# Optimization experiments

Hardware: AMD Instinct MI355X
Metric: run time of the kernel (lower is better)

The kernel has to match this reference:

```python
import jax, jax.numpy as jnp
import numpy as np

NUM_HEADS = 16
KEY_SIZE = 64
MODEL = NUM_HEADS * KEY_SIZE
B, S = 4, 2048
NEG = jnp.float32(-1e9)


def alibi_bidirectional_bias(num_heads, seq_len):
    # slopes for num_heads//2 heads: 1 / x**(i+1), x = 24**(1/h)
    h = num_heads // 2
    x = 24.0 ** (1.0 / h)
    slopes = (1.0 / x ** jnp.arange(1, h + 1, dtype=jnp.float32))[:, None, None]  # [h,1,1]
    i = jnp.arange(seq_len)
    rel = (i[None, :] - i[:, None]).astype(jnp.float32)  # rel[i,j] = j - i
    # forward (causal): tril(j - i) + (-1e9 strictly above diag)
    fwd = slopes * jnp.tril(rel) + jnp.triu(jnp.full((seq_len, seq_len), NEG), k=1)
    # backward (anti-causal): triu(i - j) + (-1e9 strictly below diag)
    bwd = slopes * jnp.triu(-rel) + jnp.tril(jnp.full((seq_len, seq_len), NEG), k=-1)
    return jnp.concatenate([fwd, bwd], axis=0)  # [num_heads, S, S]


def setup_inputs() -> dict:
    key = jax.random.key(0)
    ks = jax.random.split(key, 11)
    sc = 0.02
    d = {
        "query": jax.random.normal(ks[0], (B, S, MODEL), jnp.float32),
        "key": jax.random.normal(ks[1], (B, S, MODEL), jnp.float32),
        "value": jax.random.normal(ks[2], (B, S, MODEL), jnp.float32),
        "Wq": jax.random.normal(ks[3], (MODEL, MODEL), jnp.float32) * sc,
        "bq": jnp.zeros((MODEL,), jnp.float32),
        "Wk": jax.random.normal(ks[4], (MODEL, MODEL), jnp.float32) * sc,
        "bk": jnp.zeros((MODEL,), jnp.float32),
        "Wv": jax.random.normal(ks[5], (MODEL, MODEL), jnp.float32) * sc,
        "bv": jnp.zeros((MODEL,), jnp.float32),
        "Wo": jax.random.normal(ks[6], (MODEL, MODEL), jnp.float32) * sc,
        "bo": jnp.zeros((MODEL,), jnp.float32),
    }
    return d


def reference(query, key, value, Wq, bq, Wk, bk, Wv, bv, Wo, bo):
    b, s, _ = query.shape
    H, D = NUM_HEADS, KEY_SIZE

    def proj(x, W, bias):
        return (x @ W.T + bias).reshape(b, s, H, D).transpose(0, 2, 1, 3)  # [B,H,S,D]

    q = proj(query, Wq, bq)
    k = proj(key, Wk, bk)
    v = proj(value, Wv, bv)

    bias = alibi_bidirectional_bias(H, s)  # [H,S,S], broadcasts over batch
    scores = jnp.einsum("bhqd,bhkd->bhqk", q, k) / jnp.sqrt(jnp.float32(D)) + bias
    attn = jax.nn.softmax(scores, axis=-1)
    out = jnp.einsum("bhqk,bhkd->bhqd", attn, v)
    out = out.transpose(0, 2, 1, 3).reshape(b, s, H * D)
    return out @ Wo.T + bo
```

## Files before the change

kernel.cpp:

```cpp
#include <hip/hip_runtime.h>
#include <hip/hip_bf16.h>
#include <stdint.h>

typedef unsigned short u16;
typedef __attribute__((ext_vector_type(8))) __bf16 bf16x8;
typedef __attribute__((ext_vector_type(4))) float f32x4;
typedef __attribute__((ext_vector_type(4))) unsigned int u32x4;

#define S_LEN 2048
#define NHEAD 16
#define HDIM 64
#define DMODEL 1024
#define NBATCH 4
#define MTOK (NBATCH * S_LEN)

__device__ __forceinline__ u16 f2bf(float f) {
    uint32_t u = __float_as_uint(f);
    u += 0x7fffu + ((u >> 16) & 1u);
    return (u16)(u >> 16);
}

__device__ __forceinline__ void gld_lds16(const u16* g, u16* l) {
    __builtin_amdgcn_global_load_lds(
        (const __attribute__((address_space(1))) void*)g,
        (__attribute__((address_space(3))) void*)l, 16, 0, 0);
}

__global__ __launch_bounds__(256) void cast_all(
        const float* __restrict__ q, const float* __restrict__ k, const float* __restrict__ v,
        const float* __restrict__ wq, const float* __restrict__ wk,
        const float* __restrict__ wv, const float* __restrict__ wo,
        u16* __restrict__ xq, u16* __restrict__ xk, u16* __restrict__ xv,
        u16* __restrict__ wqb, u16* __restrict__ wkb, u16* __restrict__ wvb,
        u16* __restrict__ wob) {
    size_t idx4 = (size_t)blockIdx.x * 256 + threadIdx.x;
    const float* src;
    u16* dst;
    size_t off;
    if (idx4 < (size_t)3 << 21) {
        int t = (int)(idx4 >> 21);
        off = (idx4 & ((1u << 21) - 1)) * 4;
        src = (t == 0) ? q : (t == 1) ? k : v;
        dst = (t == 0) ? xq : (t == 1) ? xk : xv;
    } else {
        size_t w = idx4 - ((size_t)3 << 21);
        int t = (int)(w >> 18);
        off = (w & ((1u << 18) - 1)) * 4;
        src = (t == 0) ? wq : (t == 1) ? wk : (t == 2) ? wv : wo;
        dst = (t == 0) ? wqb : (t == 1) ? wkb : (t == 2) ? wvb : wob;
    }
    float4 val = *(const float4*)(src + off);
    ushort4 o;
    o.x = f2bf(val.x); o.y = f2bf(val.y); o.z = f2bf(val.z); o.w = f2bf(val.w);
    *(ushort4*)(dst + off) = o;
}

#define TM 128
#define TN 128

__device__ __forceinline__ void gemm_body(const u16* __restrict__ A,
                                          const u16* __restrict__ W,
                                          const float* __restrict__ bias,
                                          void* __restrict__ outp, int mode,
                                          int m0, int n0) {
    __shared__ __align__(16) u16 As[TM * 32];
    __shared__ __align__(16) u16 Bs[TN * 32];
    const int tid  = threadIdx.x;
    const int lane = tid & 63;
    const int wv   = tid >> 6;
    const int l16  = lane & 15;
    const int quad = lane >> 4;
    const int wm   = (wv >> 1) * 64;
    const int wn   = (wv & 1) * 64;

    f32x4 acc[4][4];
#pragma unroll
    for (int i = 0; i < 4; i++)
#pragma unroll
        for (int j = 0; j < 4; j++) acc[i][j] = {};

    const int arow = wv * 16 + (lane >> 2);
    const int acol = (lane & 3) * 8;
    const u16* gA = A + (size_t)(m0 + arow) * DMODEL + acol;
    const u16* gB = W + (size_t)(n0 + arow) * DMODEL + acol;
    u16* lA = As + wv * 16 * 32;
    u16* lB = Bs + wv * 16 * 32;

    for (int kb = 0; kb < DMODEL; kb += 32) {
        gld_lds16(gA + kb, lA);
        gld_lds16(gA + kb + (size_t)64 * DMODEL, lA + 64 * 32);
        gld_lds16(gB + kb, lB);
        gld_lds16(gB + kb + (size_t)64 * DMODEL, lB + 64 * 32);
        __builtin_amdgcn_s_waitcnt(0x0F70);
        __syncthreads();

        bf16x8 af[4], bfv[4];
#pragma unroll
        for (int i = 0; i < 4; i++)
            af[i] = *(const bf16x8*)(&As[(wm + i * 16 + l16) * 32 + quad * 8]);
#pragma unroll
        for (int j = 0; j < 4; j++)
            bfv[j] = *(const bf16x8*)(&Bs[(wn + j * 16 + l16) * 32 + quad * 8]);
#pragma unroll
        for (int i = 0; i < 4; i++)
#pragma unroll
            for (int j = 0; j < 4; j++)
                acc[i][j] = __builtin_amdgcn_mfma_f32_16x16x32_bf16(af[i], bfv[j], acc[i][j], 0, 0, 0);
        __syncthreads();
    }

#pragma unroll
    for (int j = 0; j < 4; j++) {
        int n = n0 + wn + j * 16 + l16;
        float bv = bias[n];
#pragma unroll
        for (int i = 0; i < 4; i++) {
            int mbase = m0 + wm + i * 16 + quad * 4;
#pragma unroll
            for (int r = 0; r < 4; r++) {
                int m = mbase + r;
                float v = acc[i][j][r] + bv;
                if (mode == 2) {
                    ((float*)outp)[(size_t)m * DMODEL + n] = v;
                } else {
                    int b = m >> 11, s = m & (S_LEN - 1);
                    int h = n >> 6, d = n & 63;
                    u16* o = (u16*)outp;
                    size_t idx = (mode == 0)
                        ? ((((size_t)(b * NHEAD + h)) * S_LEN + s) * HDIM + d)
                        : ((((size_t)(b * NHEAD + h)) * HDIM + d) * S_LEN + s);
                    o[idx] = f2bf(v);
                }
            }
        }
    }
}

__device__ __forceinline__ void gemm_coords(int& m0, int& n0) {
    const int lid = blockIdx.x + 8 * blockIdx.y;
    const int xcd = lid & 7;
    const int s   = lid >> 3;
    n0 = (s & 7) * TN;
    m0 = ((s >> 3) + 8 * xcd) * TM;
}

__global__ __launch_bounds__(256) void gemm_qkv(
        const u16* __restrict__ xq, const u16* __restrict__ xk, const u16* __restrict__ xv,
        const u16* __restrict__ wq, const u16* __restrict__ wk, const u16* __restrict__ wv,
        const float* __restrict__ bq, const float* __restrict__ bk, const float* __restrict__ bv,
        u16* __restrict__ Qb, u16* __restrict__ Kb, u16* __restrict__ Vb) {
    int z = blockIdx.z;
    const u16* A   = (z == 0) ? xq : (z == 1) ? xk : xv;
    const u16* W   = (z == 0) ? wq : (z == 1) ? wk : wv;
    const float* b = (z == 0) ? bq : (z == 1) ? bk : bv;
    u16* out       = (z == 0) ? Qb : (z == 1) ? Kb : Vb;
    int m0, n0;
    gemm_coords(m0, n0);
    gemm_body(A, W, b, out, (z == 2) ? 1 : 0, m0, n0);
}

__global__ __launch_bounds__(256) void gemm_one(
        const u16* __restrict__ A, const u16* __restrict__ W,
        const float* __restrict__ bias, void* __restrict__ out, int mode) {
    int m0, n0;
    gemm_coords(m0, n0);
    gemm_body(A, W, bias, out, mode, m0, n0);
}

__global__ __launch_bounds__(256, 4) void flash_kernel(
        const u16* __restrict__ Q, const u16* __restrict__ K,
        const u16* __restrict__ Vt, u16* __restrict__ AO) {
    __shared__ __align__(16) u16 Ksm[2][64 * 64];
    __shared__ __align__(16) u16 Vsm[2][64 * 64];
    __shared__ __align__(16) u16 Psm[4][16 * 64];

    const int tid  = threadIdx.x;
    const int wv   = tid >> 6;
    const int lane = tid & 63;
    const int l16  = lane & 15;
    const int quad = lane >> 4;

    const int lid   = blockIdx.x + 16 * blockIdx.y;
    const int xcd   = lid & 7;
    const int slot  = lid >> 3;
    const int bh    = xcd + 8 * (slot >> 4);
    const int g_idx = slot & 15;

    const int h    = bh & (NHEAD - 1);
    const int b    = bh >> 4;
    const bool fwd = (h < 8);
    const int sgn  = fwd ? 1 : -1;
    const float slope2 = __builtin_amdgcn_exp2f(-(float)((h & 7) + 1) * 0.5731203125901445f)
                         * 1.4426950408889634f;
    const float cL = 0.18033688011112042f;

    const u16* Kg = K + (size_t)bh * S_LEN * HDIM;
    const u16* Vg = Vt + (size_t)bh * HDIM * S_LEN;

    const int sr = lane >> 3;
    const int sc = (lane & 7) ^ sr;
    const int r0 = 16 * wv;

    const int cA = quad ^ (l16 & 7);
    const int cB = (quad + 4) ^ (l16 & 7);

    float brt[4][4];
#pragma unroll
    for (int t = 0; t < 4; t++)
#pragma unroll
        for (int r = 0; r < 4; r++)
            brt[t][r] = slope2 * (float)(sgn * (16 * t + l16 - (quad * 4 + r))) - 16.0f;

    int poff[4][4];
#pragma unroll
    for (int r = 0; r < 4; r++) {
        const int prow = quad * 4 + r;
        const int pr7  = prow & 7;
#pragma unroll
        for (int t = 0; t < 4; t++)
            poff[r][t] = prow * 64 + (((2 * t + (l16 >> 3)) ^ pr7) * 8) + (l16 & 7);
    }

    bf16x8 ones;
#pragma unroll
    for (int j = 0; j < 8; j++) ones[j] = (__bf16)1.0f;

    const float dkq = slope2 * (float)(sgn * 64);

#pragma unroll 1
    for (int half = 0; half < 2; half++) {
        const int g  = half ? (31 - g_idx) : g_idx;
        const int q0 = g * 64 + wv * 16;
        const u16* Qp = Q + ((size_t)bh * S_LEN + q0) * HDIM;
        const bf16x8 aq0 = *(const bf16x8*)(Qp + l16 * HDIM + quad * 8);
        const bf16x8 aq1 = *(const bf16x8*)(Qp + l16 * HDIM + 32 + quad * 8);

        f32x4 o[4], osum = {};
#pragma unroll
        for (int dt = 0; dt < 4; dt++) o[dt] = {};

        const int kt0 = fwd ? 0 : g;
        const int kt1 = fwd ? g : (S_LEN / 64 - 1);

        __syncthreads();
        const u16* kg = Kg + ((size_t)(kt0 * 64) + r0 + sr) * 64 + sc * 8;
        const u16* vg = Vg + (size_t)(r0 + sr) * S_LEN + kt0 * 64 + sc * 8;
        gld_lds16(kg,              &Ksm[0][r0 * 64]);
        gld_lds16(kg + 8 * 64,     &Ksm[0][(r0 + 8) * 64]);
        gld_lds16(vg,              &Vsm[0][r0 * 64]);
        gld_lds16(vg + 8 * S_LEN,  &Vsm[0][(r0 + 8) * 64]);
        kg += 64 * 64;
        vg += 64;

        float kq = slope2 * (float)(sgn * (kt0 * 64 - q0));

        int buf = 0;
        for (int kt = kt0; kt <= kt1; ++kt) {
            __builtin_amdgcn_s_waitcnt(0x0F70);
            __syncthreads();
            if (kt < kt1) {
                gld_lds16(kg,             &Ksm[buf ^ 1][r0 * 64]);
                gld_lds16(kg + 8 * 64,    &Ksm[buf ^ 1][(r0 + 8) * 64]);
                gld_lds16(vg,             &Vsm[buf ^ 1][r0 * 64]);
                gld_lds16(vg + 8 * S_LEN, &Vsm[buf ^ 1][(r0 + 8) * 64]);
                kg += 64 * 64;
                vg += 64;
            }
            const u16* Ks = &Ksm[buf][0];
            const u16* Vs = &Vsm[buf][0];

            f32x4 st[4];
#pragma unroll
            for (int t = 0; t < 4; t++) {
                const u16* kp = Ks + (16 * t + l16) * 64;
                bf16x8 k0 = *(const bf16x8*)(kp + cA * 8);
                bf16x8 k1 = *(const bf16x8*)(kp + cB * 8);
                f32x4 c = {};
                c = __builtin_amdgcn_mfma_f32_16x16x32_bf16(aq0, k0, c, 0, 0, 0);
                c = __builtin_amdgcn_mfma_f32_16x16x32_bf16(aq1, k1, c, 0, 0, 0);
                st[t] = c;
            }

            float p[4][4];
            if (kt == g) {
#pragma unroll
                for (int r = 0; r < 4; r++) {
                    const int qg = q0 + quad * 4 + r;
#pragma unroll
                    for (int t = 0; t < 4; t++) {
                        const int kg2 = kt * 64 + 16 * t + l16;
                        const bool ok = fwd ? (kg2 <= qg) : (kg2 >= qg);
                        float s2 = fmaf(st[t][r], cL, brt[t][r] + kq);
                        p[t][r] = ok ? __builtin_amdgcn_exp2f(s2) : 0.0f;
                    }
                }
            } else {
#pragma unroll
                for (int r = 0; r < 4; r++)
#pragma unroll
                    for (int t = 0; t < 4; t++)
                        p[t][r] = __builtin_amdgcn_exp2f(fmaf(st[t][r], cL, brt[t][r] + kq));
            }
            kq += dkq;

            u16* Pw = &Psm[wv][0];
#pragma unroll
            for (int r = 0; r < 4; r++)
#pragma unroll
                for (int t = 0; t < 4; t++)
                    Pw[poff[r][t]] = f2bf(p[t][r]);
            __builtin_amdgcn_s_waitcnt(0xC07F);
            bf16x8 pf0 = *(const bf16x8*)(&Pw[l16 * 64 + cA * 8]);
            bf16x8 pf1 = *(const bf16x8*)(&Pw[l16 * 64 + cB * 8]);

#pragma unroll
            for (int dt = 0; dt < 4; dt++) {
                const u16* vp = Vs + (dt * 16 + l16) * 64;
                bf16x8 v0 = *(const bf16x8*)(vp + cA * 8);
                bf16x8 v1 = *(const bf16x8*)(vp + cB * 8);
                o[dt] = __builtin_amdgcn_mfma_f32_16x16x32_bf16(pf0, v0, o[dt], 0, 0, 0);
                o[dt] = __builtin_amdgcn_mfma_f32_16x16x32_bf16(pf1, v1, o[dt], 0, 0, 0);
            }
            osum = __builtin_amdgcn_mfma_f32_16x16x32_bf16(pf0, ones, osum, 0, 0, 0);
            osum = __builtin_amdgcn_mfma_f32_16x16x32_bf16(pf1, ones, osum, 0, 0, 0);
            buf ^= 1;
        }

#pragma unroll
        for (int r = 0; r < 4; r++) {
            float inv = 1.0f / osum[r];
            int qg = q0 + quad * 4 + r;
            u16* op = AO + ((size_t)b * S_LEN + qg) * DMODEL + h * HDIM;
#pragma unroll
            for (int dt = 0; dt < 4; dt++)
                op[dt * 16 + l16] = f2bf(o[dt][r] * inv);
        }
    }
}

extern "C" void kernel_launch(void* const* d_in, const int* in_sizes, int n_in,
                              void* d_out, int out_size, void* d_ws, size_t ws_size,
                              hipStream_t stream) {
    const float* query = (const float*)d_in[0];
    const float* key   = (const float*)d_in[1];
    const float* value = (const float*)d_in[2];
    const float* Wq    = (const float*)d_in[3];
    const float* bq    = (const float*)d_in[4];
    const float* Wk    = (const float*)d_in[5];
    const float* bk    = (const float*)d_in[6];
    const float* Wv    = (const float*)d_in[7];
    const float* bv    = (const float*)d_in[8];
    const float* Wo    = (const float*)d_in[9];
    const float* bo    = (const float*)d_in[10];

    const size_t Xe = (size_t)MTOK * DMODEL;
    const size_t We = (size_t)DMODEL * DMODEL;
    u16* xq  = (u16*)d_ws;
    u16* xk  = xq + Xe;
    u16* xv  = xk + Xe;
    u16* wqb = xv + Xe;
    u16* wkb = wqb + We;
    u16* wvb = wkb + We;
    u16* wob = wvb + We;
    u16* Qb  = wob + We;
    u16* Kb  = Qb + Xe;
    u16* Vb  = Kb + Xe;
    u16* AO  = Vb + Xe;

    cast_all<<<dim3(28672), dim3(256), 0, stream>>>(
        query, key, value, Wq, Wk, Wv, Wo,
        xq, xk, xv, wqb, wkb, wvb, wob);

    gemm_qkv<<<dim3(DMODEL / TN, MTOK / TM, 3), dim3(256), 0, stream>>>(
        xq, xk, xv, wqb, wkb, wvb, bq, bk, bv, Qb, Kb, Vb);

    flash_kernel<<<dim3(16, NBATCH * NHEAD), dim3(256), 0, stream>>>(Qb, Kb, Vb, AO);

    gemm_one<<<dim3(DMODEL / TN, MTOK / TM, 1), dim3(256), 0, stream>>>(AO, wob, bo, d_out, 2);
}
```

Baseline: 334.9 us.

## Process two query tiles per wave in flash kernel and swizzle GEMM LDS

The flash kernel now gives each wave two 16-row query tiles 64 rows apart, so every K/V tile loaded into LDS is reused for twice the query work. The grid is halved and the P scratch buffer doubled to match, with per-tile activity flags so masked blocks are skipped, and the launch bound drops from 4 to 3 waves per SIMD. Separately, the GEMM LDS layout gets an XOR swizzle on the column chunk to cut bank conflicts on the fragment reads. The costs are more registers, lower occupancy, and half as many blocks to spread across the CUs.

Result: slower. 379.9 us (+13.4%).

```diff
diff --git a/kernel.cpp b/kernel.cpp
--- a/kernel.cpp
+++ b/kernel.cpp
@@ -80,11 +80,13 @@
         for (int j = 0; j < 4; j++) acc[i][j] = {};
 
     const int arow = wv * 16 + (lane >> 2);
-    const int acol = (lane & 3) * 8;
+    const int acol = ((lane & 3) ^ ((lane >> 3) & 3)) * 8;
     const u16* gA = A + (size_t)(m0 + arow) * DMODEL + acol;
     const u16* gB = W + (size_t)(n0 + arow) * DMODEL + acol;
     u16* lA = As + wv * 16 * 32;
     u16* lB = Bs + wv * 16 * 32;
+
+    const int swz = (l16 >> 1) & 3;
 
     for (int kb = 0; kb < DMODEL; kb += 32) {
         gld_lds16(gA + kb, lA);
@@ -97,10 +99,10 @@
         bf16x8 af[4], bfv[4];
 #pragma unroll
         for (int i = 0; i < 4; i++)
-            af[i] = *(const bf16x8*)(&As[(wm + i * 16 + l16) * 32 + quad * 8]);
+            af[i] = *(const bf16x8*)(&As[(wm + i * 16 + l16) * 32 + (quad ^ swz) * 8]);
 #pragma unroll
         for (int j = 0; j < 4; j++)
-            bfv[j] = *(const bf16x8*)(&Bs[(wn + j * 16 + l16) * 32 + quad * 8]);
+            bfv[j] = *(const bf16x8*)(&Bs[(wn + j * 16 + l16) * 32 + (quad ^ swz) * 8]);
 #pragma unroll
         for (int i = 0; i < 4; i++)
 #pragma unroll
@@ -167,12 +169,46 @@
     gemm_body(A, W, bias, out, mode, m0, n0);
 }
 
-__global__ __launch_bounds__(256, 4) void flash_kernel(
+__device__ __forceinline__ void exp_write(const f32x4* st, float kq, float sl16,
+        bool diag, bool fwd, int md, u16* __restrict__ Pw,
+        const int (*poff)[4], const float* br) {
+    const float cL = 0.18033688011112042f;
+    float kqt[4];
+#pragma unroll
+    for (int t = 0; t < 4; t++) kqt[t] = kq + (float)t * sl16;
+#pragma unroll
+    for (int r = 0; r < 4; r++) {
+#pragma unroll
+        for (int t = 0; t < 4; t++) {
+            float p = __builtin_amdgcn_exp2f(fmaf(st[t][r], cL, kqt[t] + br[r]));
+            if (diag) {
+                bool ok = fwd ? (16 * t - r <= md) : (16 * t - r >= md);
+                p = ok ? p : 0.0f;
+            }
+            Pw[poff[r][t]] = f2bf(p);
+        }
+    }
+}
+
+__device__ __forceinline__ void flash_epilogue(const f32x4* o, const f32x4& osum,
+        int q0, int b, int h, int quad, int l16, u16* __restrict__ AO) {
+#pragma unroll
+    for (int r = 0; r < 4; r++) {
+        float inv = 1.0f / osum[r];
+        int qg = q0 + quad * 4 + r;
+        u16* op = AO + ((size_t)b * S_LEN + qg) * DMODEL + h * HDIM;
+#pragma unroll
+        for (int dt = 0; dt < 4; dt++)
+            op[dt * 16 + l16] = f2bf(o[dt][r] * inv);
+    }
+}
+
+__global__ __launch_bounds__(256, 3) void flash_kernel(
         const u16* __restrict__ Q, const u16* __restrict__ K,
         const u16* __restrict__ Vt, u16* __restrict__ AO) {
     __shared__ __align__(16) u16 Ksm[2][64 * 64];
     __shared__ __align__(16) u16 Vsm[2][64 * 64];
-    __shared__ __align__(16) u16 Psm[4][16 * 64];
+    __shared__ __align__(16) u16 Psm[4][2][16 * 64];
 
     const int tid  = threadIdx.x;
     const int wv   = tid >> 6;
@@ -180,22 +216,22 @@
     const int l16  = lane & 15;
     const int quad = lane >> 4;
 
-    const int lid   = blockIdx.x + 16 * blockIdx.y;
+    const int lid   = blockIdx.x + 8 * blockIdx.y;
     const int xcd   = lid & 7;
     const int slot  = lid >> 3;
-    const int bh    = xcd + 8 * (slot >> 4);
-    const int g_idx = slot & 15;
+    const int bh    = xcd + 8 * (slot >> 3);
+    const int j_idx = slot & 7;
 
     const int h    = bh & (NHEAD - 1);
     const int b    = bh >> 4;
     const bool fwd = (h < 8);
-    const int sgn  = fwd ? 1 : -1;
-    const float slope2 = __builtin_amdgcn_exp2f(-(float)((h & 7) + 1) * 0.5731203125901445f)
-                         * 1.4426950408889634f;
-    const float cL = 0.18033688011112042f;
-
-    const u16* Kg = K + (size_t)bh * S_LEN * HDIM;
-    const u16* Vg = Vt + (size_t)bh * HDIM * S_LEN;
+    const float sgnf = fwd ? 1.0f : -1.0f;
+    const float sl = __builtin_amdgcn_exp2f(-(float)((h & 7) + 1) * 0.5731203125901445f)
+                     * 1.4426950408889634f * sgnf;
+    const float sl16 = sl * 16.0f;
+
+    const u16* Kg0 = K + (size_t)bh * S_LEN * HDIM;
+    const u16* Vg0 = Vt + (size_t)bh * HDIM * S_LEN;
 
     const int sr = lane >> 3;
     const int sc = (lane & 7) ^ sr;
@@ -204,12 +240,9 @@
     const int cA = quad ^ (l16 & 7);
     const int cB = (quad + 4) ^ (l16 & 7);
 
-    float brt[4][4];
-#pragma unroll
-    for (int t = 0; t < 4; t++)
-#pragma unroll
-        for (int r = 0; r < 4; r++)
-            brt[t][r] = slope2 * (float)(sgn * (16 * t + l16 - (quad * 4 + r))) - 16.0f;
+    float br[4];
+#pragma unroll
+    for (int r = 0; r < 4; r++) br[r] = sl * (float)(l16 - quad * 4 - r);
 
     int poff[4][4];
 #pragma unroll
@@ -225,34 +258,37 @@
 #pragma unroll
     for (int j = 0; j < 8; j++) ones[j] = (__bf16)1.0f;
 
-    const float dkq = slope2 * (float)(sgn * 64);
-
 #pragma unroll 1
     for (int half = 0; half < 2; half++) {
-        const int g  = half ? (31 - g_idx) : g_idx;
-        const int q0 = g * 64 + wv * 16;
-        const u16* Qp = Q + ((size_t)bh * S_LEN + q0) * HDIM;
-        const bf16x8 aq0 = *(const bf16x8*)(Qp + l16 * HDIM + quad * 8);
-        const bf16x8 aq1 = *(const bf16x8*)(Qp + l16 * HDIM + 32 + quad * 8);
-
-        f32x4 o[4], osum = {};
-#pragma unroll
-        for (int dt = 0; dt < 4; dt++) o[dt] = {};
-
-        const int kt0 = fwd ? 0 : g;
-        const int kt1 = fwd ? g : (S_LEN / 64 - 1);
+        const int J  = half ? (15 - j_idx) : j_idx;
+        const int q0a = J * 128 + wv * 16;
+        const int q0b = q0a + 64;
+        const u16* Qp = Q + ((size_t)bh * S_LEN + q0a) * HDIM;
+        const bf16x8 aq0a = *(const bf16x8*)(Qp + l16 * HDIM + quad * 8);
+        const bf16x8 aq1a = *(const bf16x8*)(Qp + l16 * HDIM + 32 + quad * 8);
+        const bf16x8 aq0b = *(const bf16x8*)(Qp + (64 + l16) * HDIM + quad * 8);
+        const bf16x8 aq1b = *(const bf16x8*)(Qp + (64 + l16) * HDIM + 32 + quad * 8);
+
+        f32x4 oA[4], oB[4], osA = {}, osB = {};
+#pragma unroll
+        for (int dt = 0; dt < 4; dt++) { oA[dt] = {}; oB[dt] = {}; }
+
+        const int dga = 2 * J, dgb = 2 * J + 1;
+        const int kt0 = fwd ? 0 : dga;
+        const int kt1 = fwd ? dgb : (S_LEN / 64 - 1);
 
         __syncthreads();
-        const u16* kg = Kg + ((size_t)(kt0 * 64) + r0 + sr) * 64 + sc * 8;
-        const u16* vg = Vg + (size_t)(r0 + sr) * S_LEN + kt0 * 64 + sc * 8;
-        gld_lds16(kg,              &Ksm[0][r0 * 64]);
-        gld_lds16(kg + 8 * 64,     &Ksm[0][(r0 + 8) * 64]);
-        gld_lds16(vg,              &Vsm[0][r0 * 64]);
-        gld_lds16(vg + 8 * S_LEN,  &Vsm[0][(r0 + 8) * 64]);
+        const u16* kg = Kg0 + ((size_t)(kt0 * 64) + r0 + sr) * 64 + sc * 8;
+        const u16* vg = Vg0 + (size_t)(r0 + sr) * S_LEN + kt0 * 64 + sc * 8;
+        gld_lds16(kg,             &Ksm[0][r0 * 64]);
+        gld_lds16(kg + 8 * 64,    &Ksm[0][(r0 + 8) * 64]);
+        gld_lds16(vg,             &Vsm[0][r0 * 64]);
+        gld_lds16(vg + 8 * S_LEN, &Vsm[0][(r0 + 8) * 64]);
         kg += 64 * 64;
         vg += 64;
 
-        float kq = slope2 * (float)(sgn * (kt0 * 64 - q0));
+        float kqa = sl * (float)(kt0 * 64 - q0a) - 16.0f;
+        float kqb = kqa - sl * 64.0f;
 
         int buf = 0;
         for (int kt = kt0; kt <= kt1; ++kt) {
@@ -269,72 +305,77 @@
             const u16* Ks = &Ksm[buf][0];
             const u16* Vs = &Vsm[buf][0];
 
-            f32x4 st[4];
+            const bool actA = fwd ? (kt <= dga) : true;
+            const bool actB = fwd ? true : (kt >= dgb);
+
+            f32x4 stA[4], stB[4];
 #pragma unroll
             for (int t = 0; t < 4; t++) {
                 const u16* kp = Ks + (16 * t + l16) * 64;
                 bf16x8 k0 = *(const bf16x8*)(kp + cA * 8);
                 bf16x8 k1 = *(const bf16x8*)(kp + cB * 8);
-                f32x4 c = {};
-                c = __builtin_amdgcn_mfma_f32_16x16x32_bf16(aq0, k0, c, 0, 0, 0);
-                c = __builtin_amdgcn_mfma_f32_16x16x32_bf16(aq1, k1, c, 0, 0, 0);
-                st[t] = c;
-            }
-
-            float p[4][4];
-            if (kt == g) {
-#pragma unroll
-                for (int r = 0; r < 4; r++) {
-                    const int qg = q0 + quad * 4 + r;
-#pragma unroll
-                    for (int t = 0; t < 4; t++) {
-                        const int kg2 = kt * 64 + 16 * t + l16;
-                        const bool ok = fwd ? (kg2 <= qg) : (kg2 >= qg);
-                        float s2 = fmaf(st[t][r], cL, brt[t][r] + kq);
-                        p[t][r] = ok ? __builtin_amdgcn_exp2f(s2) : 0.0f;
-                    }
+                if (actA) {
+                    f32x4 c = {};
+                    c = __builtin_amdgcn_mfma_f32_16x16x32_bf16(aq0a, k0, c, 0, 0, 0);
+                    c = __builtin_amdgcn_mfma_f32_16x16x32_bf16(aq1a, k1, c, 0, 0, 0);
+                    stA[t] = c;
                 }
-            } else {
-#pragma unroll
-                for (int r = 0; r < 4; r++)
-#pragma unroll
-                    for (int t = 0; t < 4; t++)
-                        p[t][r] = __builtin_amdgcn_exp2f(fmaf(st[t][r], cL, brt[t][r] + kq));
-            }
-            kq += dkq;
-
-            u16* Pw = &Psm[wv][0];
-#pragma unroll
-            for (int r = 0; r < 4; r++)
-#pragma unroll
-                for (int t = 0; t < 4; t++)
-                    Pw[poff[r][t]] = f2bf(p[t][r]);
+                if (actB) {
+                    f32x4 c = {};
+                    c = __builtin_amdgcn_mfma_f32_16x16x32_bf16(aq0b, k0, c, 0, 0, 0);
+                    c = __builtin_amdgcn_mfma_f32_16x16x32_bf16(aq1b, k1, c, 0, 0, 0);
+                    stB[t] = c;
+                }
+            }
+
+            if (actA)
+                exp_write(stA, kqa, sl16, kt == dga, fwd,
+                          q0a + quad * 4 - kt * 64 - l16, &Psm[wv][0][0], poff, br);
+            if (actB)
+                exp_write(stB, kqb, sl16, kt == dgb, fwd,
+                          q0b + quad * 4 - kt * 64 - l16, &Psm[wv][1][0], poff, br);
             __builtin_amdgcn_s_waitcnt(0xC07F);
-            bf16x8 pf0 = *(const bf16x8*)(&Pw[l16 * 64 + cA * 8]);
-            bf16x8 pf1 = *(const bf16x8*)(&Pw[l16 * 64 + cB * 8]);
+
+            bf16x8 pfA0, pfA1, pfB0, pfB1;
+            if (actA) {
+                pfA0 = *(const bf16x8*)(&Psm[wv][0][l16 * 64 + cA * 8]);
+                pfA1 = *(const bf16x8*)(&Psm[wv][0][l16 * 64 + cB * 8]);
+            }
+            if (actB) {
+                pfB0 = *(const bf16x8*)(&Psm[wv][1][l16 * 64 + cA * 8]);
+                pfB1 = *(const bf16x8*)(&Psm[wv][1][l16 * 64 + cB * 8]);
+            }
 
 #pragma unroll
             for (int dt = 0; dt < 4; dt++) {
                 const u16* vp = Vs + (dt * 16 + l16) * 64;
                 bf16x8 v0 = *(const bf16x8*)(vp + cA * 8);
                 bf16x8 v1 = *(const bf16x8*)(vp + cB * 8);
-                o[dt] = __builtin_amdgcn_mfma_f32_16x16x32_bf16(pf0, v0, o[dt], 0, 0, 0);
-                o[dt] = __builtin_amdgcn_mfma_f32_16x16x32_bf16(pf1, v1, o[dt], 0, 0, 0);
-            }
-            osum = __builtin_amdgcn_mfma_f32_16x16x32_bf16(pf0, ones, osum, 0, 0, 0);
-            osum = __builtin_amdgcn_mfma_f32_16x16x32_bf16(pf1, ones, osum, 0, 0, 0);
+                if (actA) {
+                    oA[dt] = __builtin_amdgcn_mfma_f32_16x16x32_bf16(pfA0, v0, oA[dt], 0, 0, 0);
+                    oA[dt] = __builtin_amdgcn_mfma_f32_16x16x32_bf16(pfA1, v1, oA[dt], 0, 0, 0);
+                }
+                if (actB) {
+                    oB[dt] = __builtin_amdgcn_mfma_f32_16x16x32_bf16(pfB0, v0, oB[dt], 0, 0, 0);
+                    oB[dt] = __builtin_amdgcn_mfma_f32_16x16x32_bf16(pfB1, v1, oB[dt], 0, 0, 0);
+                }
+            }
+            if (actA) {
+                osA = __builtin_amdgcn_mfma_f32_16x16x32_bf16(pfA0, ones, osA, 0, 0, 0);
+                osA = __builtin_amdgcn_mfma_f32_16x16x32_bf16(pfA1, ones, osA, 0, 0, 0);
+            }
+            if (actB) {
+                osB = __builtin_amdgcn_mfma_f32_16x16x32_bf16(pfB0, ones, osB, 0, 0, 0);
+                osB = __builtin_amdgcn_mfma_f32_16x16x32_bf16(pfB1, ones, osB, 0, 0, 0);
+            }
+
+            kqa += sl * 64.0f;
+            kqb += sl * 64.0f;
             buf ^= 1;
         }
 
-#pragma unroll
-        for (int r = 0; r < 4; r++) {
-            float inv = 1.0f / osum[r];
-            int qg = q0 + quad * 4 + r;
-            u16* op = AO + ((size_t)b * S_LEN + qg) * DMODEL + h * HDIM;
-#pragma unroll
-            for (int dt = 0; dt < 4; dt++)
-                op[dt * 16 + l16] = f2bf(o[dt][r] * inv);
-        }
+        flash_epilogue(oA, osA, q0a, b, h, quad, l16, AO);
+        flash_epilogue(oB, osB, q0b, b, h, quad, l16, AO);
     }
 }
 
@@ -374,7 +415,7 @@
     gemm_qkv<<<dim3(DMODEL / TN, MTOK / TM, 3), dim3(256), 0, stream>>>(
         xq, xk, xv, wqb, wkb, wvb, bq, bk, bv, Qb, Kb, Vb);
 
-    flash_kernel<<<dim3(16, NBATCH * NHEAD), dim3(256), 0, stream>>>(Qb, Kb, Vb, AO);
+    flash_kernel<<<dim3(8, NBATCH * NHEAD), dim3(256), 0, stream>>>(Qb, Kb, Vb, AO);
 
     gemm_one<<<dim3(DMODEL / TN, MTOK / TM, 1), dim3(256), 0, stream>>>(AO, wob, bo, d_out, 2);
 }
```
